# Kernel tuning notes

Measured on AMD Instinct MI355X. Metric: run time of the kernel, lower is better.

Reference implementation:

```python
import jax, jax.numpy as jnp
import numpy as np

ROUTING_ITERS = 3


def squash(v):
    # v: [..., D]; l2norm over last dim
    l2 = jnp.linalg.norm(v, axis=-1, keepdims=True)
    unit = v / l2
    factor = (l2 * l2) / (1.0 + l2 * l2)
    return unit * factor


def setup_inputs() -> dict:
    key = jax.random.key(0)
    k1, k2 = jax.random.split(key)
    B, N_in, D_in = 256, 1152, 8
    N_out, D_out = 10, 16
    x = jax.random.normal(k1, (B, N_in, D_in), dtype=jnp.float32)
    W = jax.random.normal(k2, (N_in, N_out, D_out, D_in), dtype=jnp.float32)
    return {"x": x, "W": W}


def reference(x, W):
    # x: [B, N_in, D_in], W: [N_in, N_out, D_out, D_in]
    # u_hat[b,i,o,:] = W[i,o] @ x[b,i]
    u_hat = jnp.einsum('iodk,bik->biod', W, x)  # [B, N_in, N_out, D_out]
    N_in, N_out = W.shape[0], W.shape[1]
    b_logits = jnp.zeros((N_in, N_out), dtype=x.dtype)
    s = None
    for r in range(ROUTING_ITERS + 1):
        c = jax.nn.softmax(b_logits, axis=-1)            # [N_in, N_out]
        s = jnp.einsum('io,biod->bod', c, u_hat)          # [B, N_out, D_out]
        s = squash(s)
        if r < ROUTING_ITERS:
            # agreement summed over batch (matches original .sum(dim=0))
            b_logits = b_logits + jnp.einsum('biod,bod->io', u_hat, s)
    return s
```

## Files before the change

kernel.cpp:

```cpp
#include <hip/hip_runtime.h>
#include <math.h>

typedef __attribute__((ext_vector_type(8))) short bf16x8;
typedef __attribute__((ext_vector_type(4))) float f32x4;
typedef unsigned short u16;
typedef unsigned int u32;

#define NI    1152
#define DI    8
#define NO    10
#define DOUT  16
#define F     160
#define KTOT  9216
#define KS    288
#define SK    72

#define OFF_SFH 0
#define OFF_SFL 20480
#define OFF_P   40960
#define OFF_BA  2990080
#define OFF_BB  3001600
#define OFF_TP  3013120

union U8 { u16 u[8]; uint4 v; bf16x8 b; };

__device__ inline u16 bf16hi(float x) {
    u32 u = __float_as_uint(x);
    return (u16)((u + 0x7FFFu + ((u >> 16) & 1u)) >> 16);
}
__device__ inline float bf2f(u16 h) { return __uint_as_float(((u32)h) << 16); }

__device__ inline void split8(const float* v, bf16x8* bh, bf16x8* bl) {
    U8 h, l;
#pragma unroll
    for (int j = 0; j < 8; j++) {
        u16 hh = bf16hi(v[j]);
        h.u[j] = hh;
        l.u[j] = bf16hi(v[j] - bf2f(hh));
    }
    *bh = h.b; *bl = l.b;
}

__global__ __launch_bounds__(256) void s_round(const float* __restrict__ x,
                                               const float* __restrict__ W,
                                               const float* __restrict__ tpart,
                                               const float* __restrict__ blogIn,
                                               float* __restrict__ blogOut,
                                               float* __restrict__ P, int mode) {
    __shared__ __attribute__((aligned(16))) u16 cwhS[10240];
    __shared__ __attribute__((aligned(16))) u16 cwlS[10240];
    __shared__ float ts[16][NO];
    __shared__ float cls[16][NO];

    const int t = threadIdx.x, l = t & 63, w = t >> 6;
    const int bid = blockIdx.x;
    const int sk  = bid % SK;
    const int fh  = (bid / SK) & 1;
    const int btg = bid / (2 * SK);

    if (mode == 0) {
        if (t < 160) cls[t / NO][t % NO] = 0.1f;
    } else {
        if (t < 160) {
            int il = t / NO, o = t % NO;
            int ig = sk * 16 + il;
            float a = tpart[(size_t)ig * NO + o] +
                      tpart[(size_t)(NI + ig) * NO + o] +
                      tpart[(size_t)(2 * NI + ig) * NO + o] +
                      tpart[(size_t)(3 * NI + ig) * NO + o];
            float bnew = (mode == 2 ? blogIn[ig * NO + o] : 0.f) + a;
            blogOut[ig * NO + o] = bnew;
            ts[il][o] = bnew;
        }
        __syncthreads();
        if (t < 16) {
            float m = -3.402823466e+38f;
#pragma unroll
            for (int o = 0; o < NO; o++) m = fmaxf(m, ts[t][o]);
            float e[NO];
            float sum = 0.f;
#pragma unroll
            for (int o = 0; o < NO; o++) { e[o] = expf(ts[t][o] - m); sum += e[o]; }
            float inv = 1.f / sum;
#pragma unroll
            for (int o = 0; o < NO; o++) cls[t][o] = e[o] * inv;
        }
    }
    __syncthreads();

#pragma unroll
    for (int p = 0; p < 5; p++) {
        int vid  = p * 256 + t;
        int frag = vid >> 6;
        int ll   = vid & 63;
        int n = frag >> 2, kk = frag & 3;
        int ks = sk * 4 + kk;
        int o  = fh * 5 + n;
        int i  = ks * 4 + (ll >> 4), d = ll & 15;
        float cv = cls[kk * 4 + (ll >> 4)][o];
        const float* wp = W + ((size_t)(i * NO + o) * DOUT + d) * DI;
        float4 a = ((const float4*)wp)[0];
        float4 b = ((const float4*)wp)[1];
        float v[8] = {cv*a.x, cv*a.y, cv*a.z, cv*a.w, cv*b.x, cv*b.y, cv*b.z, cv*b.w};
        U8 ph, pl;
#pragma unroll
        for (int j = 0; j < 8; j++) {
            u16 h = bf16hi(v[j]);
            ph.u[j] = h; pl.u[j] = bf16hi(v[j] - bf2f(h));
        }
        *(uint4*)(cwhS + frag * 512 + ll * 8) = ph.v;
        *(uint4*)(cwlS + frag * 512 + ll * 8) = pl.v;
    }
    __syncthreads();

    const int bt = btg * 4 + w;
    f32x4 z = {0.f, 0.f, 0.f, 0.f};
    f32x4 acc[5];
#pragma unroll
    for (int n = 0; n < 5; n++) acc[n] = z;

#pragma unroll
    for (int kk = 0; kk < 4; kk++) {
        int ks = sk * 4 + kk;
        const float* xp = x + (size_t)(bt * 16 + (l & 15)) * KTOT + ks * 32 + (l >> 4) * 8;
        float4 a4 = ((const float4*)xp)[0];
        float4 b4 = ((const float4*)xp)[1];
        float v[8] = {a4.x, a4.y, a4.z, a4.w, b4.x, b4.y, b4.z, b4.w};
        bf16x8 ah, al;
        split8(v, &ah, &al);
#pragma unroll
        for (int n = 0; n < 5; n++) {
            bf16x8 bh = *(const bf16x8*)(cwhS + (n * 4 + kk) * 512 + l * 8);
            bf16x8 bl = *(const bf16x8*)(cwlS + (n * 4 + kk) * 512 + l * 8);
            acc[n] = __builtin_amdgcn_mfma_f32_16x16x32_bf16(ah, bh, acc[n], 0, 0, 0);
            acc[n] = __builtin_amdgcn_mfma_f32_16x16x32_bf16(ah, bl, acc[n], 0, 0, 0);
            acc[n] = __builtin_amdgcn_mfma_f32_16x16x32_bf16(al, bh, acc[n], 0, 0, 0);
        }
    }
    const int c0 = l & 15, rg = l >> 4;
    float* Pp = P + (size_t)sk * 40960 + (size_t)(bt * 16 + rg * 4) * F + fh * 80 + c0;
#pragma unroll
    for (int n = 0; n < 5; n++)
#pragma unroll
        for (int rr = 0; rr < 4; rr++)
            Pp[(size_t)rr * F + n * 16] = acc[n][rr];
}

__global__ void rs(const float* __restrict__ P, float* __restrict__ sout,
                   u16* __restrict__ sfh, u16* __restrict__ sfl, int last) {
    int idx = blockIdx.x * 256 + threadIdx.x;
    float sum = 0.f;
#pragma unroll 8
    for (int sk2 = 0; sk2 < SK; sk2++) sum += P[(size_t)sk2 * 40960 + idx];
    float n2 = sum * sum;
#pragma unroll
    for (int off = 8; off > 0; off >>= 1) n2 += __shfl_xor(n2, off, 16);
    float l2v = sqrtf(n2);
    float scale = l2v / (1.f + n2);
    float sv = sum * scale;
    if (last) {
        sout[idx] = sv;
    } else {
        int b = idx / F, f = idx % F;
        size_t si = (size_t)((f >> 4) * 8 + (b >> 5)) * 512 +
                    (size_t)(((b >> 3) & 3) * 16 + (f & 15)) * 8 + (b & 7);
        u16 h = bf16hi(sv);
        sfh[si] = h;
        sfl[si] = bf16hi(sv - bf2f(h));
    }
}

__global__ __launch_bounds__(256) void c1(const u16* __restrict__ sfh,
                                          const u16* __restrict__ sfl,
                                          const float* __restrict__ x,
                                          const float* __restrict__ W,
                                          float* __restrict__ tpart) {
    __shared__ __attribute__((aligned(16))) float G[160 * 68];
    const int t = threadIdx.x, l = t & 63, w = t >> 6;
    const int nb = blockIdx.x >> 2, bq = blockIdx.x & 3;
    const int wm = w & 1, wn = w >> 1;

    f32x4 z = {0.f, 0.f, 0.f, 0.f};
    f32x4 acc[5][2];
#pragma unroll
    for (int m = 0; m < 5; m++)
#pragma unroll
        for (int n = 0; n < 2; n++) acc[m][n] = z;

#pragma unroll
    for (int ksl = 0; ksl < 2; ksl++) {
        int ksb = bq * 2 + ksl;
        bf16x8 ah[5], al[5];
#pragma unroll
        for (int m = 0; m < 5; m++) {
            size_t ai = ((size_t)((wm * 5 + m) * 8 + ksb)) * 512 + l * 8;
            ah[m] = *(const bf16x8*)(sfh + ai);
            al[m] = *(const bf16x8*)(sfl + ai);
        }
#pragma unroll
        for (int nl = 0; nl < 2; nl++) {
            int ns = nb * 4 + wn * 2 + nl;
            const float* xp = x + (size_t)(ksb * 32 + (l >> 4) * 8) * KTOT + ns * 16 + (l & 15);
            float v[8];
#pragma unroll
            for (int j = 0; j < 8; j++) v[j] = xp[(size_t)j * KTOT];
            bf16x8 bh, blo;
            split8(v, &bh, &blo);
#pragma unroll
            for (int m = 0; m < 5; m++) {
                acc[m][nl] = __builtin_amdgcn_mfma_f32_16x16x32_bf16(ah[m], bh, acc[m][nl], 0, 0, 0);
                acc[m][nl] = __builtin_amdgcn_mfma_f32_16x16x32_bf16(ah[m], blo, acc[m][nl], 0, 0, 0);
                acc[m][nl] = __builtin_amdgcn_mfma_f32_16x16x32_bf16(al[m], bh, acc[m][nl], 0, 0, 0);
            }
        }
    }
    const int c0 = l & 15, rg = l >> 4;
#pragma unroll
    for (int m = 0; m < 5; m++)
#pragma unroll
        for (int nl = 0; nl < 2; nl++)
#pragma unroll
            for (int rr = 0; rr < 4; rr++)
                G[(wm * 80 + m * 16 + rg * 4 + rr) * 68 + wn * 32 + nl * 16 + c0] = acc[m][nl][rr];
    __syncthreads();
    if (t < 160) {
        int i_l = t / 20, o = (t % 20) >> 1, dh = t & 1;
        int i_g = nb * 8 + i_l;
        const float* wp = W + (size_t)(i_g * NO + o) * 128 + dh * 64;
        float sum = 0.f;
#pragma unroll
        for (int d = 0; d < 8; d++) {
            const float* gp = &G[(o * 16 + dh * 8 + d) * 68 + i_l * 8];
            float4 g0 = ((const float4*)gp)[0], g1 = ((const float4*)gp)[1];
            float4 w0 = ((const float4*)(wp + d * 8))[0], w1 = ((const float4*)(wp + d * 8))[1];
            sum += g0.x * w0.x + g0.y * w0.y + g0.z * w0.z + g0.w * w0.w +
                   g1.x * w1.x + g1.y * w1.y + g1.z * w1.z + g1.w * w1.w;
        }
        sum += __shfl_xor(sum, 1);
        if (dh == 0) tpart[(size_t)(bq * NI + i_g) * NO + o] = sum;
    }
}

extern "C" void kernel_launch(void* const* d_in, const int* in_sizes, int n_in,
                              void* d_out, int out_size, void* d_ws, size_t ws_size,
                              hipStream_t stream) {
    const float* x = (const float*)d_in[0];
    const float* W = (const float*)d_in[1];
    float* out = (float*)d_out;
    float* ws  = (float*)d_ws;
    u16* sfh = (u16*)(ws + OFF_SFH);
    u16* sfl = (u16*)(ws + OFF_SFL);
    float* P   = ws + OFF_P;
    float* blA = ws + OFF_BA;
    float* blB = ws + OFF_BB;
    float* tp  = ws + OFF_TP;

    for (int r = 0; r < 4; r++) {
        int mode = (r == 0) ? 0 : (r == 1 ? 1 : 2);
        const float* bIn = (r == 2) ? blB : blA;
        float* bOut      = (r == 2) ? blA : blB;
        s_round<<<576, 256, 0, stream>>>(x, W, tp, bIn, bOut, P, mode);
        rs<<<160, 256, 0, stream>>>(P, out, sfh, sfl, r == 3 ? 1 : 0);
        if (r < 3)
            c1<<<576, 256, 0, stream>>>(sfh, sfl, x, W, tp);
    }
}
```

Before: 98.33 us.

## Halve split-K partitions in s_round, loop two K tiles per block

Each s_round block now covers eight k-slices in two staged LDS tiles instead of four, so split-K partitions drop from 72 to 36 and the grid from 576 to 288 blocks. This halves the partial-sum buffer P that rs must write and read back. Partial-sum stores and loads become nontemporal, and the last round skips writing blog logits it never uses. The cost is fewer blocks on the GPU and an extra barrier pair per tile inside each block.

New measurement: 104.2 us. 1.06x slower.

```diff
diff --git a/kernel.cpp b/kernel.cpp
--- a/kernel.cpp
+++ b/kernel.cpp
@@ -13,14 +13,14 @@
 #define F     160
 #define KTOT  9216
 #define KS    288
-#define SK    72
+#define SK    36
 
 #define OFF_SFH 0
 #define OFF_SFL 20480
 #define OFF_P   40960
-#define OFF_BA  2990080
-#define OFF_BB  3001600
-#define OFF_TP  3013120
+#define OFF_BA  1515520
+#define OFF_BB  1527040
+#define OFF_TP  1538560
 
 union U8 { u16 u[8]; uint4 v; bf16x8 b; };
 
@@ -46,11 +46,11 @@
                                                const float* __restrict__ tpart,
                                                const float* __restrict__ blogIn,
                                                float* __restrict__ blogOut,
-                                               float* __restrict__ P, int mode) {
+                                               float* __restrict__ P, int r) {
     __shared__ __attribute__((aligned(16))) u16 cwhS[10240];
     __shared__ __attribute__((aligned(16))) u16 cwlS[10240];
-    __shared__ float ts[16][NO];
-    __shared__ float cls[16][NO];
+    __shared__ float ts[32][NO];
+    __shared__ float cls[32][NO];
 
     const int t = threadIdx.x, l = t & 63, w = t >> 6;
     const int bid = blockIdx.x;
@@ -58,22 +58,22 @@
     const int fh  = (bid / SK) & 1;
     const int btg = bid / (2 * SK);
 
-    if (mode == 0) {
-        if (t < 160) cls[t / NO][t % NO] = 0.1f;
+    if (r == 0) {
+        for (int e = t; e < 320; e += 256) cls[e / NO][e % NO] = 0.1f;
     } else {
-        if (t < 160) {
-            int il = t / NO, o = t % NO;
-            int ig = sk * 16 + il;
+        for (int e = t; e < 320; e += 256) {
+            int il = e / NO, o = e % NO;
+            int ig = sk * 32 + il;
             float a = tpart[(size_t)ig * NO + o] +
                       tpart[(size_t)(NI + ig) * NO + o] +
                       tpart[(size_t)(2 * NI + ig) * NO + o] +
                       tpart[(size_t)(3 * NI + ig) * NO + o];
-            float bnew = (mode == 2 ? blogIn[ig * NO + o] : 0.f) + a;
-            blogOut[ig * NO + o] = bnew;
+            float bnew = (r >= 2 ? blogIn[ig * NO + o] : 0.f) + a;
+            if (r < 3) blogOut[ig * NO + o] = bnew;
             ts[il][o] = bnew;
         }
         __syncthreads();
-        if (t < 16) {
+        if (t < 32) {
             float m = -3.402823466e+38f;
 #pragma unroll
             for (int o = 0; o < NO; o++) m = fmaxf(m, ts[t][o]);
@@ -86,32 +86,6 @@
             for (int o = 0; o < NO; o++) cls[t][o] = e[o] * inv;
         }
     }
-    __syncthreads();
-
-#pragma unroll
-    for (int p = 0; p < 5; p++) {
-        int vid  = p * 256 + t;
-        int frag = vid >> 6;
-        int ll   = vid & 63;
-        int n = frag >> 2, kk = frag & 3;
-        int ks = sk * 4 + kk;
-        int o  = fh * 5 + n;
-        int i  = ks * 4 + (ll >> 4), d = ll & 15;
-        float cv = cls[kk * 4 + (ll >> 4)][o];
-        const float* wp = W + ((size_t)(i * NO + o) * DOUT + d) * DI;
-        float4 a = ((const float4*)wp)[0];
-        float4 b = ((const float4*)wp)[1];
-        float v[8] = {cv*a.x, cv*a.y, cv*a.z, cv*a.w, cv*b.x, cv*b.y, cv*b.z, cv*b.w};
-        U8 ph, pl;
-#pragma unroll
-        for (int j = 0; j < 8; j++) {
-            u16 h = bf16hi(v[j]);
-            ph.u[j] = h; pl.u[j] = bf16hi(v[j] - bf2f(h));
-        }
-        *(uint4*)(cwhS + frag * 512 + ll * 8) = ph.v;
-        *(uint4*)(cwlS + frag * 512 + ll * 8) = pl.v;
-    }
-    __syncthreads();
 
     const int bt = btg * 4 + w;
     f32x4 z = {0.f, 0.f, 0.f, 0.f};
@@ -120,21 +94,50 @@
     for (int n = 0; n < 5; n++) acc[n] = z;
 
 #pragma unroll
-    for (int kk = 0; kk < 4; kk++) {
-        int ks = sk * 4 + kk;
-        const float* xp = x + (size_t)(bt * 16 + (l & 15)) * KTOT + ks * 32 + (l >> 4) * 8;
-        float4 a4 = ((const float4*)xp)[0];
-        float4 b4 = ((const float4*)xp)[1];
-        float v[8] = {a4.x, a4.y, a4.z, a4.w, b4.x, b4.y, b4.z, b4.w};
-        bf16x8 ah, al;
-        split8(v, &ah, &al);
-#pragma unroll
-        for (int n = 0; n < 5; n++) {
-            bf16x8 bh = *(const bf16x8*)(cwhS + (n * 4 + kk) * 512 + l * 8);
-            bf16x8 bl = *(const bf16x8*)(cwlS + (n * 4 + kk) * 512 + l * 8);
-            acc[n] = __builtin_amdgcn_mfma_f32_16x16x32_bf16(ah, bh, acc[n], 0, 0, 0);
-            acc[n] = __builtin_amdgcn_mfma_f32_16x16x32_bf16(ah, bl, acc[n], 0, 0, 0);
-            acc[n] = __builtin_amdgcn_mfma_f32_16x16x32_bf16(al, bh, acc[n], 0, 0, 0);
+    for (int kt = 0; kt < 2; kt++) {
+        __syncthreads();
+#pragma unroll
+        for (int p = 0; p < 5; p++) {
+            int vid  = p * 256 + t;
+            int frag = vid >> 6;
+            int ll   = vid & 63;
+            int n = frag >> 2, kkl = frag & 3;
+            int ksl = kt * 4 + kkl;
+            int ks  = sk * 8 + ksl;
+            int o   = fh * 5 + n;
+            int i   = ks * 4 + (ll >> 4), d = ll & 15;
+            float cv = cls[ksl * 4 + (ll >> 4)][o];
+            const float* wp = W + ((size_t)(i * NO + o) * DOUT + d) * DI;
+            float4 a = ((const float4*)wp)[0];
+            float4 b = ((const float4*)wp)[1];
+            float v[8] = {cv*a.x, cv*a.y, cv*a.z, cv*a.w, cv*b.x, cv*b.y, cv*b.z, cv*b.w};
+            U8 ph, pl;
+#pragma unroll
+            for (int j = 0; j < 8; j++) {
+                u16 h = bf16hi(v[j]);
+                ph.u[j] = h; pl.u[j] = bf16hi(v[j] - bf2f(h));
+            }
+            *(uint4*)(cwhS + frag * 512 + ll * 8) = ph.v;
+            *(uint4*)(cwlS + frag * 512 + ll * 8) = pl.v;
+        }
+        __syncthreads();
+#pragma unroll
+        for (int kkl = 0; kkl < 4; kkl++) {
+            int ks = sk * 8 + kt * 4 + kkl;
+            const float* xp = x + (size_t)(bt * 16 + (l & 15)) * KTOT + ks * 32 + (l >> 4) * 8;
+            float4 a4 = ((const float4*)xp)[0];
+            float4 b4 = ((const float4*)xp)[1];
+            float v[8] = {a4.x, a4.y, a4.z, a4.w, b4.x, b4.y, b4.z, b4.w};
+            bf16x8 ah, al;
+            split8(v, &ah, &al);
+#pragma unroll
+            for (int n = 0; n < 5; n++) {
+                bf16x8 bh = *(const bf16x8*)(cwhS + (n * 4 + kkl) * 512 + l * 8);
+                bf16x8 bl = *(const bf16x8*)(cwlS + (n * 4 + kkl) * 512 + l * 8);
+                acc[n] = __builtin_amdgcn_mfma_f32_16x16x32_bf16(ah, bh, acc[n], 0, 0, 0);
+                acc[n] = __builtin_amdgcn_mfma_f32_16x16x32_bf16(ah, bl, acc[n], 0, 0, 0);
+                acc[n] = __builtin_amdgcn_mfma_f32_16x16x32_bf16(al, bh, acc[n], 0, 0, 0);
+            }
         }
     }
     const int c0 = l & 15, rg = l >> 4;
@@ -143,15 +146,17 @@
     for (int n = 0; n < 5; n++)
 #pragma unroll
         for (int rr = 0; rr < 4; rr++)
-            Pp[(size_t)rr * F + n * 16] = acc[n][rr];
+            __builtin_nontemporal_store(acc[n][rr], Pp + (size_t)rr * F + n * 16);
 }
 
 __global__ void rs(const float* __restrict__ P, float* __restrict__ sout,
                    u16* __restrict__ sfh, u16* __restrict__ sfl, int last) {
     int idx = blockIdx.x * 256 + threadIdx.x;
+    const float* pp = P + idx;
     float sum = 0.f;
-#pragma unroll 8
-    for (int sk2 = 0; sk2 < SK; sk2++) sum += P[(size_t)sk2 * 40960 + idx];
+#pragma unroll 6
+    for (int sk2 = 0; sk2 < SK; sk2++)
+        sum += __builtin_nontemporal_load(pp + (size_t)sk2 * 40960);
     float n2 = sum * sum;
 #pragma unroll
     for (int off = 8; off > 0; off >>= 1) n2 += __shfl_xor(n2, off, 16);
@@ -256,10 +261,9 @@
     float* tp  = ws + OFF_TP;
 
     for (int r = 0; r < 4; r++) {
-        int mode = (r == 0) ? 0 : (r == 1 ? 1 : 2);
         const float* bIn = (r == 2) ? blB : blA;
         float* bOut      = (r == 2) ? blA : blB;
-        s_round<<<576, 256, 0, stream>>>(x, W, tp, bIn, bOut, P, mode);
+        s_round<<<288, 256, 0, stream>>>(x, W, tp, bIn, bOut, P, r);
         rs<<<160, 256, 0, stream>>>(P, out, sfh, sfl, r == 3 ? 1 : 0);
         if (r < 3)
             c1<<<576, 256, 0, stream>>>(sfh, sfl, x, W, tp);
```
